# Kernel tuning notes

Hardware: AMD Instinct MI355X
Metric: run time of the kernel (lower is better)

Reference implementation:

```python
import jax, jax.numpy as jnp
import numpy as np

N = 100000   # nodes
E = 1600000  # edges
F_IN = 128   # node_features
H = 64       # hidden_features


def setup_inputs() -> dict:
    key = jax.random.key(0)
    ks = jax.random.split(key, 16)
    s = 0.05
    return {
        "x": jax.random.normal(ks[0], (N, F_IN), dtype=jnp.float32),
        "edge_index": jax.random.randint(ks[1], (2, E), 0, N, dtype=jnp.int64),
        "W1": jax.random.normal(ks[2], (H, F_IN), dtype=jnp.float32) * s,
        "b1": jnp.zeros((H,), dtype=jnp.float32),
        "W2": jax.random.normal(ks[3], (H, H), dtype=jnp.float32) * s,
        "b2": jnp.zeros((H,), dtype=jnp.float32),
        "Wk": jax.random.normal(ks[4], (H, H), dtype=jnp.float32) * s,
        "bk": jnp.zeros((H,), dtype=jnp.float32),
        "Wq": jax.random.normal(ks[5], (H, H), dtype=jnp.float32) * s,
        "bq": jnp.zeros((H,), dtype=jnp.float32),
        "Wv": jax.random.normal(ks[6], (H, H), dtype=jnp.float32) * s,
        "bv": jnp.zeros((H,), dtype=jnp.float32),
        "Ws": jax.random.normal(ks[7], (H, H), dtype=jnp.float32) * s,  # lin_skip, bias=False
        "b_gate": jnp.zeros((H,), dtype=jnp.float32),                   # conv bias param
        "Wsc": jax.random.normal(ks[8], (1, H), dtype=jnp.float32) * s,
        "bsc": jnp.zeros((1,), dtype=jnp.float32),
    }


def reference(x, edge_index, W1, b1, W2, b2, Wk, bk, Wq, bq, Wv, bv, Ws, b_gate, Wsc, bsc):
    # MLP front-end: Linear + ReLU + Linear
    h = jax.nn.relu(x @ W1.T + b1)
    h = h @ W2.T + b2                      # [N, H]

    # ResGatedGraphConv (sum aggregation, sigmoid gating)
    k = h @ Wk.T + bk                      # key on destination nodes
    q = h @ Wq.T + bq                      # query on source nodes
    v = h @ Wv.T + bv                      # value on source nodes

    src = edge_index[0]                    # j
    dst = edge_index[1]                    # i
    # message_ij = sigmoid(k_i + q_j) * v_j, scatter-add to destination i
    msg = jax.nn.sigmoid(k[dst] + q[src]) * v[src]   # [E, H]
    agg = jax.ops.segment_sum(msg, dst, num_segments=N)

    out = agg + h @ Ws.T + b_gate          # root skip (no bias) + conv bias

    # scorer head
    score = out @ Wsc.T + bsc              # [N, 1]
    return score
```

## Files before the change

### kernel.cpp

```cpp
#include <hip/hip_runtime.h>

#define HD  64
#define FIN 128

#define WS_W1H   0
#define WS_W1L   4096
#define WS_MALL  8192
#define WS_BK    14848
#define WS_BQ    14912
#define WS_BVW   14976
#define WS_BASE  15040
#define WS_REC   15104

#define C1f  3.9026344e-3f
#define C3f  (-7.67612e-8f)
#define C5f  1.2236660e-12f

typedef __attribute__((ext_vector_type(8))) short short8;
typedef __attribute__((ext_vector_type(4))) float f32x4;

__device__ __forceinline__ unsigned bf16rne(float f) {
    unsigned u = __float_as_uint(f);
    unsigned r = ((u >> 16) & 1u) + 0x7fffu;
    return (u + r) >> 16;
}
__device__ __forceinline__ float blo(unsigned u) { return __uint_as_float(u << 16); }
__device__ __forceinline__ float bhi(unsigned u) { return __uint_as_float(u & 0xffff0000u); }

__device__ __forceinline__ float grp4(unsigned ku, unsigned qu, unsigned va,
                                      unsigned vb, float p) {
    #pragma unroll
    for (int i = 0; i < 4; ++i) {
        float kf = (float)((ku >> (8 * i)) & 255u);
        float qf = (float)((qu >> (8 * i)) & 255u);
        unsigned vu = (i < 2) ? va : vb;
        float vf = (i & 1) ? bhi(vu) : blo(vu);
        float xx = kf + qf;
        xx = fminf(fmaxf(xx, 128.f), 384.f);
        float sv = xx - 256.f;
        float z = sv * sv;
        float w = fmaf(z, C5f, C3f);
        w = fmaf(z, w, C1f);
        p = fmaf(vf * sv, w, p);
        p = fmaf(vf, 0.5f, p);
    }
    return p;
}

__global__ void gnn_prep(const float* __restrict__ W1, const float* __restrict__ W2,
                         const float* __restrict__ b2,
                         const float* __restrict__ Wk, const float* __restrict__ bk,
                         const float* __restrict__ Wq, const float* __restrict__ bq,
                         const float* __restrict__ Wv, const float* __restrict__ bv,
                         const float* __restrict__ Wsm, const float* __restrict__ Wsc,
                         const float* __restrict__ bgate, const float* __restrict__ bsc,
                         float* __restrict__ ws) {
    __shared__ float w2s[4096];
    __shared__ float wxsT[65 * 64];
    int b = blockIdx.x, t = threadIdx.x;
    unsigned short* w1h  = (unsigned short*)(ws + WS_W1H);
    unsigned short* w1l  = (unsigned short*)(ws + WS_W1L);
    unsigned short* mall = (unsigned short*)(ws + WS_MALL);
    if (b == 0) {
        for (int idx = t; idx < HD * FIN; idx += blockDim.x) {
            float v = W1[idx];
            unsigned u = __float_as_uint(v);
            w1h[idx] = (unsigned short)(u >> 16);
            float rem = v - __uint_as_float(u & 0xffff0000u);
            w1l[idx] = (unsigned short)bf16rne(rem);
        }
    } else if (b <= 12) {
        int m = (b - 1) >> 2, qtr = (b - 1) & 3;
        const float* Wx = (m == 0) ? Wk : (m == 1) ? Wq : Wv;
        const float* bx = (m == 0) ? bk : (m == 1) ? bq : bv;
        int boff = (m == 0) ? WS_BK : (m == 1) ? WS_BQ : WS_BVW;
        for (int i = t * 4; i < 4096; i += 1024)
            *(float4*)&w2s[i] = *(const float4*)&W2[i];
        for (int idx = t; idx < 4096; idx += 256) {
            int o = idx >> 6, c = idx & 63;
            wxsT[c * 65 + o] = Wx[idx];
        }
        __syncthreads();
        for (int idx = t; idx < 1024; idx += 256) {
            int a = qtr * 16 + (idx >> 6), o = idx & 63;
            float acc = 0.f;
            for (int c = 0; c < HD; ++c) acc += w2s[c * HD + a] * wxsT[c * 65 + o];
            if (m == 2) acc *= Wsc[o];
            mall[(m * 64 + o) * HD + a] = (unsigned short)bf16rne(acc);
        }
        if (qtr == 0 && t < HD) {
            float acc = bx[t];
            for (int c = 0; c < HD; ++c) acc += b2[c] * wxsT[c * 65 + t];
            if (m == 2) acc *= Wsc[t];
            ws[boff + t] = acc;
        }
    } else {
        __shared__ float wsk[HD];
        if (t < HD) {
            float a = 0.f;
            for (int d = 0; d < HD; ++d) a += Wsm[d * HD + t] * Wsc[d];
            wsk[t] = a;
        }
        __syncthreads();
        if (t < HD) {
            float a = 0.f;
            for (int c = 0; c < HD; ++c) a += W2[c * HD + t] * wsk[c];
            mall[192 * HD + t] = (unsigned short)bf16rne(a);
        }
        for (int idx = t; idx < 15 * HD; idx += 256)
            mall[193 * HD + idx] = 0;
        if (t == 0) {
            float a = bsc[0];
            for (int d = 0; d < HD; ++d) a += bgate[d] * Wsc[d];
            float acc2 = 0.f;
            __syncthreads();
            for (int c = 0; c < HD; ++c) {
                float wk2 = 0.f;
                for (int d = 0; d < HD; ++d) wk2 += Wsm[d * HD + c] * Wsc[d];
                acc2 += b2[c] * wk2;
            }
            ws[WS_BASE] = a + acc2;
        }
    }
}

__global__ __launch_bounds__(256, 3) void gnn_node(const float* __restrict__ x,
                                                   const float* __restrict__ b1,
                                                   const float* __restrict__ ws,
                                                   unsigned* __restrict__ nodebuf,
                                                   float* __restrict__ score, int N) {
    __shared__ __align__(16) char smem[32768];
    char* XHb = smem;
    char* XLb = smem + 16384;

    int tid = threadIdx.x;
    int l = tid & 63, w = tid >> 6;
    int nbase = blockIdx.x * 64;

    #pragma unroll
    for (int it = 0; it < 8; ++it) {
        int idx = it * 64 + l;
        int nl = 16 * w + (idx >> 5);
        int c4 = idx & 31;
        int node = min(nbase + nl, N - 1);
        float4 v = ((const float4*)x)[(size_t)node * 32 + c4];
        unsigned u0 = __float_as_uint(v.x), u1 = __float_as_uint(v.y);
        unsigned u2 = __float_as_uint(v.z), u3 = __float_as_uint(v.w);
        uint2 hx, lx;
        hx.x = (u0 >> 16) | (u1 & 0xffff0000u);
        hx.y = (u2 >> 16) | (u3 & 0xffff0000u);
        float r0 = v.x - __uint_as_float(u0 & 0xffff0000u);
        float r1 = v.y - __uint_as_float(u1 & 0xffff0000u);
        float r2 = v.z - __uint_as_float(u2 & 0xffff0000u);
        float r3 = v.w - __uint_as_float(u3 & 0xffff0000u);
        lx.x = bf16rne(r0) | (bf16rne(r1) << 16);
        lx.y = bf16rne(r2) | (bf16rne(r3) << 16);
        int bo = (nl * 256 + c4 * 8) ^ ((nl & 7) << 4);
        *(uint2*)(XHb + bo) = hx;
        *(uint2*)(XLb + bo) = lx;
    }
    __syncthreads();

    int rl = l & 15, kb = l >> 4;
    int rowA = 16 * w + rl;
    int swzA = (rowA & 7) << 4;

    const unsigned short* w1h = (const unsigned short*)(ws + WS_W1H);
    const unsigned short* w1l = (const unsigned short*)(ws + WS_W1L);
    f32x4 acc1[4];
    #pragma unroll
    for (int t = 0; t < 4; ++t) {
        float bv = b1[t * 16 + rl];
        acc1[t] = (f32x4){bv, bv, bv, bv};
    }
    #pragma unroll
    for (int s = 0; s < 4; ++s) {
        int abyte = (rowA * 256 + s * 64 + kb * 16) ^ swzA;
        short8 ah = *(const short8*)(XHb + abyte);
        short8 al = *(const short8*)(XLb + abyte);
        int koff = s * 32 + kb * 8;
        #pragma unroll
        for (int t = 0; t < 4; ++t) {
            int col = t * 16 + rl;
            short8 bh = *(const short8*)&w1h[col * FIN + koff];
            short8 bl = *(const short8*)&w1l[col * FIN + koff];
            acc1[t] = __builtin_amdgcn_mfma_f32_16x16x32_bf16(ah, bh, acc1[t], 0, 0, 0);
            acc1[t] = __builtin_amdgcn_mfma_f32_16x16x32_bf16(al, bh, acc1[t], 0, 0, 0);
            acc1[t] = __builtin_amdgcn_mfma_f32_16x16x32_bf16(ah, bl, acc1[t], 0, 0, 0);
        }
    }
    __syncthreads();

    int r0w = (l >> 4) * 4;
    #pragma unroll
    for (int t = 0; t < 4; ++t) {
        int col = t * 16 + rl;
        #pragma unroll
        for (int r = 0; r < 4; ++r) {
            int row = 16 * w + r0w + r;
            float v = fmaxf(acc1[t][r], 0.f);
            int hb = (row * 128 + col * 2) ^ ((row & 7) << 4);
            *(unsigned short*)(smem + hb) = (unsigned short)bf16rne(v);
        }
    }
    __syncthreads();

    const unsigned short* mall = (const unsigned short*)(ws + WS_MALL);
    const float* bK = ws + WS_BK;
    const float* bQ = ws + WS_BQ;
    const float* bV = ws + WS_BVW;
    float base = ws[WS_BASE];
    f32x4 acc2[13];
    #pragma unroll
    for (int t = 0; t < 4; ++t) {
        float v = bK[t * 16 + rl];
        acc2[t] = (f32x4){v, v, v, v};
    }
    #pragma unroll
    for (int t = 0; t < 4; ++t) {
        float v = bQ[t * 16 + rl];
        acc2[4 + t] = (f32x4){v, v, v, v};
    }
    #pragma unroll
    for (int t = 0; t < 4; ++t) {
        float v = bV[t * 16 + rl];
        acc2[8 + t] = (f32x4){v, v, v, v};
    }
    acc2[12] = (f32x4){0.f, 0.f, 0.f, 0.f};

    #pragma unroll
    for (int s = 0; s < 2; ++s) {
        int abyte = (rowA * 128 + (s * 32 + kb * 8) * 2) ^ swzA;
        short8 a = *(const short8*)(smem + abyte);
        int koff = s * 32 + kb * 8;
        #pragma unroll
        for (int t = 0; t < 13; ++t) {
            short8 b = *(const short8*)&mall[(t * 16 + rl) * HD + koff];
            acc2[t] = __builtin_amdgcn_mfma_f32_16x16x32_bf16(a, b, acc2[t], 0, 0, 0);
        }
    }

    char* Ku = smem + 16384;
    char* Qu = smem + 20480;
    char* VW = smem + 24576;
    #pragma unroll
    for (int t = 0; t < 4; ++t) {
        int col = t * 16 + rl;
        #pragma unroll
        for (int r = 0; r < 4; ++r) {
            int row = 16 * w + r0w + r;
            int ek = min(max(__float2int_rn(fmaf(acc2[t][r],     64.f, 128.f)), 0), 255);
            int eq = min(max(__float2int_rn(fmaf(acc2[4 + t][r], 64.f, 128.f)), 0), 255);
            Ku[row * 64 + col] = (char)ek;
            Qu[row * 64 + col] = (char)eq;
            *(unsigned short*)(VW + row * 128 + col * 2) =
                (unsigned short)bf16rne(acc2[8 + t][r]);
        }
    }
    if (rl == 0) {
        #pragma unroll
        for (int r = 0; r < 4; ++r) {
            int node = nbase + 16 * w + r0w + r;
            if (node < N) score[node] = base + acc2[12][r];
        }
    }
    __syncthreads();

    uint4* recs = (uint4*)nodebuf;
    #pragma unroll
    for (int it = 0; it < 4; ++it) {
        int c = it * 256 + tid;
        int n = c >> 4, p = c & 15;
        uint4 v;
        if (p < 4)      v = *(const uint4*)(Ku + n * 64 + p * 16);
        else if (p < 8) v = *(const uint4*)(Qu + n * 64 + (p - 4) * 16);
        else            v = *(const uint4*)(VW + n * 128 + (p - 8) * 16);
        int node = nbase + n;
        if (node < N) recs[(size_t)node * 16 + p] = v;
    }
}

__global__ __launch_bounds__(256) void gnn_edge(const int* __restrict__ ei,
                                                const uint4* __restrict__ nb,
                                                float* __restrict__ score, int E) {
    int t = blockIdx.x * 256 + threadIdx.x;
    int e = t >> 2;
    if (e >= E) return;
    int f = t & 3;
    int s = ei[e];
    int d = ei[E + e];
    uint4 ku = nb[(size_t)d * 16 + f];
    uint4 qu = nb[(size_t)s * 16 + 4 + f];
    uint4 va = nb[(size_t)s * 16 + 8 + 2 * f];
    uint4 vb = nb[(size_t)s * 16 + 9 + 2 * f];
    float p = 0.f;
    p = grp4(ku.x, qu.x, va.x, va.y, p);
    p = grp4(ku.y, qu.y, va.z, va.w, p);
    p = grp4(ku.z, qu.z, vb.x, vb.y, p);
    p = grp4(ku.w, qu.w, vb.z, vb.w, p);
    p += __shfl_down(p, 2, 4);
    p += __shfl_down(p, 1, 4);
    if (f == 0) atomicAdd(&score[d], p);
}

extern "C" void kernel_launch(void* const* d_in, const int* in_sizes, int n_in,
                              void* d_out, int out_size, void* d_ws, size_t ws_size,
                              hipStream_t stream) {
    const float* x    = (const float*)d_in[0];
    const int*   ei   = (const int*)d_in[1];
    const float* W1   = (const float*)d_in[2];
    const float* b1   = (const float*)d_in[3];
    const float* W2   = (const float*)d_in[4];
    const float* b2   = (const float*)d_in[5];
    const float* Wk   = (const float*)d_in[6];
    const float* bk   = (const float*)d_in[7];
    const float* Wq   = (const float*)d_in[8];
    const float* bq   = (const float*)d_in[9];
    const float* Wv   = (const float*)d_in[10];
    const float* bv   = (const float*)d_in[11];
    const float* Wsm  = (const float*)d_in[12];
    const float* bgat = (const float*)d_in[13];
    const float* Wsc  = (const float*)d_in[14];
    const float* bsc  = (const float*)d_in[15];

    int N = in_sizes[0] / FIN;
    int E = in_sizes[1] / 2;

    float* ws    = (float*)d_ws;
    float* recs  = ws + WS_REC;
    float* score = (float*)d_out;

    int NB = (N + 63) / 64;
    gnn_prep<<<14, 256, 0, stream>>>(W1, W2, b2, Wk, bk, Wq, bq, Wv, bv,
                                     Wsm, Wsc, bgat, bsc, ws);
    gnn_node<<<NB, 256, 0, stream>>>(x, b1, ws, (unsigned*)recs, score, N);
    gnn_edge<<<(E * 4 + 255) / 256, 256, 0, stream>>>(ei, (const uint4*)recs, score, E);
}
```

Before: 294.3 us.

## Bucket edges by source block for L2-local gathers in edge kernel

Adds a per-call histogram, scan and scatter pass that groups edges into 32 buckets by source-node range (4096 nodes each), packing dst and local src into one 32-bit word. The edge kernel then walks the buckets with blocks interleaved so each XCD-like group of blocks touches a compact source range, meant to improve cache hit rates for the q/v gathers. Node records are split into separate K and QV arrays so the dst gather and src gather hit smaller arrays. This adds three extra kernels and extra traffic to read the edge list twice and write a packed buffer.

```diff
diff --git a/kernel.cpp b/kernel.cpp
--- a/kernel.cpp
+++ b/kernel.cpp
@@ -10,7 +10,12 @@
 #define WS_BQ    14912
 #define WS_BVW   14976
 #define WS_BASE  15040
-#define WS_REC   15104
+#define WS_CNT   15104
+#define WS_BOFF  15136
+#define WS_CUR   15172
+#define WS_K     15360
+
+#define BSHIFT 12
 
 #define C1f  3.9026344e-3f
 #define C3f  (-7.67612e-8f)
@@ -73,7 +78,7 @@
         int m = (b - 1) >> 2, qtr = (b - 1) & 3;
         const float* Wx = (m == 0) ? Wk : (m == 1) ? Wq : Wv;
         const float* bx = (m == 0) ? bk : (m == 1) ? bq : bv;
-        int boff = (m == 0) ? WS_BK : (m == 1) ? WS_BQ : WS_BVW;
+        int boffw = (m == 0) ? WS_BK : (m == 1) ? WS_BQ : WS_BVW;
         for (int i = t * 4; i < 4096; i += 1024)
             *(float4*)&w2s[i] = *(const float4*)&W2[i];
         for (int idx = t; idx < 4096; idx += 256) {
@@ -92,9 +97,9 @@
             float acc = bx[t];
             for (int c = 0; c < HD; ++c) acc += b2[c] * wxsT[c * 65 + t];
             if (m == 2) acc *= Wsc[t];
-            ws[boff + t] = acc;
-        }
-    } else {
+            ws[boffw + t] = acc;
+        }
+    } else if (b == 13) {
         __shared__ float wsk[HD];
         if (t < HD) {
             float a = 0.f;
@@ -113,7 +118,6 @@
             float a = bsc[0];
             for (int d = 0; d < HD; ++d) a += bgate[d] * Wsc[d];
             float acc2 = 0.f;
-            __syncthreads();
             for (int c = 0; c < HD; ++c) {
                 float wk2 = 0.f;
                 for (int d = 0; d < HD; ++d) wk2 += Wsm[d * HD + c] * Wsc[d];
@@ -121,13 +125,16 @@
             }
             ws[WS_BASE] = a + acc2;
         }
+    } else {
+        if (t < 128) ((int*)(ws + WS_CNT))[t] = 0;
     }
 }
 
 __global__ __launch_bounds__(256, 3) void gnn_node(const float* __restrict__ x,
                                                    const float* __restrict__ b1,
                                                    const float* __restrict__ ws,
-                                                   unsigned* __restrict__ nodebuf,
+                                                   uint4* __restrict__ karr,
+                                                   uint4* __restrict__ qv,
                                                    float* __restrict__ score, int N) {
     __shared__ __align__(16) char smem[32768];
     char* XHb = smem;
@@ -266,41 +273,115 @@
     }
     __syncthreads();
 
-    uint4* recs = (uint4*)nodebuf;
-    #pragma unroll
-    for (int it = 0; it < 4; ++it) {
-        int c = it * 256 + tid;
-        int n = c >> 4, p = c & 15;
-        uint4 v;
-        if (p < 4)      v = *(const uint4*)(Ku + n * 64 + p * 16);
-        else if (p < 8) v = *(const uint4*)(Qu + n * 64 + (p - 4) * 16);
-        else            v = *(const uint4*)(VW + n * 128 + (p - 8) * 16);
+    {
+        int n = tid >> 2, p = tid & 3;
         int node = nbase + n;
-        if (node < N) recs[(size_t)node * 16 + p] = v;
-    }
-}
-
-__global__ __launch_bounds__(256) void gnn_edge(const int* __restrict__ ei,
-                                                const uint4* __restrict__ nb,
-                                                float* __restrict__ score, int E) {
-    int t = blockIdx.x * 256 + threadIdx.x;
-    int e = t >> 2;
-    if (e >= E) return;
-    int f = t & 3;
-    int s = ei[e];
-    int d = ei[E + e];
-    uint4 ku = nb[(size_t)d * 16 + f];
-    uint4 qu = nb[(size_t)s * 16 + 4 + f];
-    uint4 va = nb[(size_t)s * 16 + 8 + 2 * f];
-    uint4 vb = nb[(size_t)s * 16 + 9 + 2 * f];
-    float p = 0.f;
-    p = grp4(ku.x, qu.x, va.x, va.y, p);
-    p = grp4(ku.y, qu.y, va.z, va.w, p);
-    p = grp4(ku.z, qu.z, vb.x, vb.y, p);
-    p = grp4(ku.w, qu.w, vb.z, vb.w, p);
-    p += __shfl_down(p, 2, 4);
-    p += __shfl_down(p, 1, 4);
-    if (f == 0) atomicAdd(&score[d], p);
+        if (node < N)
+            karr[(size_t)node * 4 + p] = *(const uint4*)(Ku + n * 64 + p * 16);
+    }
+    #pragma unroll
+    for (int it = 0; it < 3; ++it) {
+        int n = tid >> 2, p = (tid & 3) + it * 4;
+        int node = nbase + n;
+        const char* srcp = (p < 4) ? (Qu + n * 64 + p * 16)
+                                   : (VW + n * 128 + (p - 4) * 16);
+        if (node < N) qv[(size_t)node * 12 + p] = *(const uint4*)srcp;
+    }
+}
+
+__global__ __launch_bounds__(256) void gnn_hist(const int* __restrict__ ei,
+                                                int* __restrict__ cnt, int E) {
+    __shared__ int lc[32];
+    int t = threadIdx.x;
+    if (t < 32) lc[t] = 0;
+    __syncthreads();
+    for (int e = blockIdx.x * 256 + t; e < E; e += gridDim.x * 256)
+        atomicAdd(&lc[ei[e] >> BSHIFT], 1);
+    __syncthreads();
+    if (t < 32 && lc[t]) atomicAdd(&cnt[t], lc[t]);
+}
+
+__global__ void gnn_scan(const int* __restrict__ cnt, int* __restrict__ boff,
+                         int* __restrict__ cur) {
+    if (threadIdx.x == 0) {
+        int s = 0;
+        for (int b = 0; b < 32; ++b) { boff[b] = s; cur[b] = s; s += cnt[b]; }
+        boff[32] = s;
+    }
+}
+
+__global__ __launch_bounds__(256) void gnn_scatter(const int* __restrict__ ei,
+                                                   int* __restrict__ cur,
+                                                   unsigned* __restrict__ ebuf, int E) {
+    __shared__ int lc[32], gb[32], lcur[32];
+    int t = threadIdx.x;
+    int base = blockIdx.x * 1024;
+    if (t < 32) lc[t] = 0;
+    __syncthreads();
+    int myb[4]; unsigned mypk[4];
+    #pragma unroll
+    for (int i = 0; i < 4; ++i) {
+        int e = base + i * 256 + t;
+        myb[i] = -1;
+        if (e < E) {
+            int src = ei[e], dst = ei[E + e];
+            myb[i] = src >> BSHIFT;
+            mypk[i] = (unsigned)dst | ((unsigned)(src & 4095) << 17);
+            atomicAdd(&lc[myb[i]], 1);
+        }
+    }
+    __syncthreads();
+    if (t < 32) {
+        gb[t] = lc[t] ? atomicAdd(&cur[t], lc[t]) : 0;
+        lcur[t] = 0;
+    }
+    __syncthreads();
+    #pragma unroll
+    for (int i = 0; i < 4; ++i) {
+        if (myb[i] >= 0) {
+            int r = atomicAdd(&lcur[myb[i]], 1);
+            ebuf[gb[myb[i]] + r] = mypk[i];
+        }
+    }
+}
+
+__global__ __launch_bounds__(256) void gnn_edge(const unsigned* __restrict__ ebuf,
+                                                const int* __restrict__ boff,
+                                                const uint4* __restrict__ karr,
+                                                const uint4* __restrict__ qv,
+                                                float* __restrict__ score,
+                                                int nb, int cpb) {
+    int bid = blockIdx.x;
+    int x = bid & 7, ci = bid >> 3;
+    int t = threadIdx.x;
+    int q = t >> 2, f = t & 3;
+    for (int sb = 0; sb < 4; ++sb) {
+        int b = x + 8 * sb;
+        if (b >= nb) break;
+        int eend = boff[b + 1];
+        for (int c = ci; ; c += cpb) {
+            int e0 = boff[b] + c * 64;
+            if (e0 >= eend) break;
+            int ge = e0 + q;
+            if (ge < eend) {
+                unsigned pk = ebuf[ge];
+                int dst = (int)(pk & 0x1FFFFu);
+                int src = (b << BSHIFT) + (int)(pk >> 17);
+                uint4 ku = karr[(size_t)dst * 4 + f];
+                uint4 qu = qv[(size_t)src * 12 + f];
+                uint4 va = qv[(size_t)src * 12 + 4 + 2 * f];
+                uint4 vb = qv[(size_t)src * 12 + 5 + 2 * f];
+                float p = 0.f;
+                p = grp4(ku.x, qu.x, va.x, va.y, p);
+                p = grp4(ku.y, qu.y, va.z, va.w, p);
+                p = grp4(ku.z, qu.z, vb.x, vb.y, p);
+                p = grp4(ku.w, qu.w, vb.z, vb.w, p);
+                p += __shfl_down(p, 2, 4);
+                p += __shfl_down(p, 1, 4);
+                if (f == 0) atomicAdd(&score[dst], p);
+            }
+        }
+    }
 }
 
 extern "C" void kernel_launch(void* const* d_in, const int* in_sizes, int n_in,
@@ -327,12 +408,26 @@
     int E = in_sizes[1] / 2;
 
     float* ws    = (float*)d_ws;
-    float* recs  = ws + WS_REC;
+    int*   cnt   = (int*)(ws + WS_CNT);
+    int*   boff  = (int*)(ws + WS_BOFF);
+    int*   cur   = (int*)(ws + WS_CUR);
+    float* karr  = ws + WS_K;
+    float* qvarr = karr + (size_t)N * 16;
+    unsigned* ebuf = (unsigned*)(qvarr + (size_t)N * 48);
     float* score = (float*)d_out;
 
     int NB = (N + 63) / 64;
-    gnn_prep<<<14, 256, 0, stream>>>(W1, W2, b2, Wk, bk, Wq, bq, Wv, bv,
+    int nb = (N + (1 << BSHIFT) - 1) >> BSHIFT;
+    long long mean = ((long long)E << BSHIFT) / N;
+    int cpb = (int)(mean * 108 / 100 / 64) + 2;
+
+    gnn_prep<<<15, 256, 0, stream>>>(W1, W2, b2, Wk, bk, Wq, bq, Wv, bv,
                                      Wsm, Wsc, bgat, bsc, ws);
-    gnn_node<<<NB, 256, 0, stream>>>(x, b1, ws, (unsigned*)recs, score, N);
-    gnn_edge<<<(E * 4 + 255) / 256, 256, 0, stream>>>(ei, (const uint4*)recs, score, E);
-}
+    gnn_node<<<NB, 256, 0, stream>>>(x, b1, ws, (uint4*)karr, (uint4*)qvarr,
+                                     score, N);
+    gnn_hist<<<1024, 256, 0, stream>>>(ei, cnt, E);
+    gnn_scan<<<1, 64, 0, stream>>>(cnt, boff, cur);
+    gnn_scatter<<<(E + 1023) / 1024, 256, 0, stream>>>(ei, cur, ebuf, E);
+    gnn_edge<<<8 * cpb, 256, 0, stream>>>(ebuf, boff, (const uint4*)karr,
+                                          (const uint4*)qvarr, score, nb, cpb);
+}
```

New measurement: 332.7 us. 1.13x slower.

## Bucket edges by source block and stage source Q/V records in LDS

Applied to the files above, without the earlier changes.

Adds an edge-binning pass, fused into the node kernel as extra blocks, that scatters each edge into a per-128-source bucket with packed dst/local-src indices, plus a spill list for overflowing buckets. The edge kernel then loads each bucket's Q/V records into shared memory once and reads only K for the destination from global memory. The node output is split into separate K and QV arrays. The aim is to cut random global gathers of source features, at the cost of an extra atomic-based scatter pass and edge-buffer traffic.

```diff
diff --git a/kernel.cpp b/kernel.cpp
--- a/kernel.cpp
+++ b/kernel.cpp
@@ -10,7 +10,13 @@
 #define WS_BQ    14912
 #define WS_BVW   14976
 #define WS_BASE  15040
-#define WS_REC   15104
+#define WS_CUR   15104
+#define WS_K     16128
+
+#define BSHIFT 7
+#define BSIZE  128
+#define CAP    2368
+#define SPILLCAP 262144
 
 #define C1f  3.9026344e-3f
 #define C3f  (-7.67612e-8f)
@@ -54,7 +60,7 @@
                          const float* __restrict__ Wv, const float* __restrict__ bv,
                          const float* __restrict__ Wsm, const float* __restrict__ Wsc,
                          const float* __restrict__ bgate, const float* __restrict__ bsc,
-                         float* __restrict__ ws) {
+                         float* __restrict__ ws, int* __restrict__ cur) {
     __shared__ float w2s[4096];
     __shared__ float wxsT[65 * 64];
     int b = blockIdx.x, t = threadIdx.x;
@@ -73,7 +79,7 @@
         int m = (b - 1) >> 2, qtr = (b - 1) & 3;
         const float* Wx = (m == 0) ? Wk : (m == 1) ? Wq : Wv;
         const float* bx = (m == 0) ? bk : (m == 1) ? bq : bv;
-        int boff = (m == 0) ? WS_BK : (m == 1) ? WS_BQ : WS_BVW;
+        int boffw = (m == 0) ? WS_BK : (m == 1) ? WS_BQ : WS_BVW;
         for (int i = t * 4; i < 4096; i += 1024)
             *(float4*)&w2s[i] = *(const float4*)&W2[i];
         for (int idx = t; idx < 4096; idx += 256) {
@@ -92,9 +98,9 @@
             float acc = bx[t];
             for (int c = 0; c < HD; ++c) acc += b2[c] * wxsT[c * 65 + t];
             if (m == 2) acc *= Wsc[t];
-            ws[boff + t] = acc;
-        }
-    } else {
+            ws[boffw + t] = acc;
+        }
+    } else if (b == 13) {
         __shared__ float wsk[HD];
         if (t < HD) {
             float a = 0.f;
@@ -113,7 +119,6 @@
             float a = bsc[0];
             for (int d = 0; d < HD; ++d) a += bgate[d] * Wsc[d];
             float acc2 = 0.f;
-            __syncthreads();
             for (int c = 0; c < HD; ++c) {
                 float wk2 = 0.f;
                 for (int d = 0; d < HD; ++d) wk2 += Wsm[d * HD + c] * Wsc[d];
@@ -121,21 +126,47 @@
             }
             ws[WS_BASE] = a + acc2;
         }
-    }
-}
-
-__global__ __launch_bounds__(256, 3) void gnn_node(const float* __restrict__ x,
-                                                   const float* __restrict__ b1,
-                                                   const float* __restrict__ ws,
-                                                   unsigned* __restrict__ nodebuf,
-                                                   float* __restrict__ score, int N) {
+    } else {
+        for (int i = t; i < 1024; i += 256) cur[i] = 0;
+    }
+}
+
+__global__ __launch_bounds__(256, 3) void gnn_nodescatter(
+        const float* __restrict__ x, const float* __restrict__ b1,
+        const float* __restrict__ ws, uint4* __restrict__ karr,
+        uint4* __restrict__ qv, float* __restrict__ score, int N,
+        const int* __restrict__ ei, int* __restrict__ cur,
+        unsigned* __restrict__ ebuf, int* __restrict__ spillS,
+        int* __restrict__ spillD, int E, int NB, int nbkt) {
+    int tid = threadIdx.x;
+    int bid = blockIdx.x;
+
+    if (bid >= NB) {
+        int base = (bid - NB) * 1024;
+        #pragma unroll
+        for (int i = 0; i < 4; ++i) {
+            int e = base + i * 256 + tid;
+            if (e < E) {
+                int src = ei[e], dst = ei[E + e];
+                int b = src >> BSHIFT;
+                int r = atomicAdd(&cur[b], 1);
+                if (r < CAP)
+                    ebuf[(size_t)b * CAP + r] =
+                        (unsigned)dst | ((unsigned)(src & (BSIZE - 1)) << 17);
+                else {
+                    int sr = atomicAdd(&cur[nbkt], 1);
+                    if (sr < SPILLCAP) { spillS[sr] = src; spillD[sr] = dst; }
+                }
+            }
+        }
+        return;
+    }
+
     __shared__ __align__(16) char smem[32768];
     char* XHb = smem;
     char* XLb = smem + 16384;
-
-    int tid = threadIdx.x;
     int l = tid & 63, w = tid >> 6;
-    int nbase = blockIdx.x * 64;
+    int nbase = bid * 64;
 
     #pragma unroll
     for (int it = 0; it < 8; ++it) {
@@ -266,41 +297,87 @@
     }
     __syncthreads();
 
-    uint4* recs = (uint4*)nodebuf;
-    #pragma unroll
-    for (int it = 0; it < 4; ++it) {
-        int c = it * 256 + tid;
-        int n = c >> 4, p = c & 15;
-        uint4 v;
-        if (p < 4)      v = *(const uint4*)(Ku + n * 64 + p * 16);
-        else if (p < 8) v = *(const uint4*)(Qu + n * 64 + (p - 4) * 16);
-        else            v = *(const uint4*)(VW + n * 128 + (p - 8) * 16);
+    {
+        int n = tid >> 2, p = tid & 3;
         int node = nbase + n;
-        if (node < N) recs[(size_t)node * 16 + p] = v;
-    }
-}
-
-__global__ __launch_bounds__(256) void gnn_edge(const int* __restrict__ ei,
-                                                const uint4* __restrict__ nb,
-                                                float* __restrict__ score, int E) {
-    int t = blockIdx.x * 256 + threadIdx.x;
-    int e = t >> 2;
-    if (e >= E) return;
-    int f = t & 3;
-    int s = ei[e];
-    int d = ei[E + e];
-    uint4 ku = nb[(size_t)d * 16 + f];
-    uint4 qu = nb[(size_t)s * 16 + 4 + f];
-    uint4 va = nb[(size_t)s * 16 + 8 + 2 * f];
-    uint4 vb = nb[(size_t)s * 16 + 9 + 2 * f];
-    float p = 0.f;
-    p = grp4(ku.x, qu.x, va.x, va.y, p);
-    p = grp4(ku.y, qu.y, va.z, va.w, p);
-    p = grp4(ku.z, qu.z, vb.x, vb.y, p);
-    p = grp4(ku.w, qu.w, vb.z, vb.w, p);
-    p += __shfl_down(p, 2, 4);
-    p += __shfl_down(p, 1, 4);
-    if (f == 0) atomicAdd(&score[d], p);
+        if (node < N)
+            karr[(size_t)node * 4 + p] = *(const uint4*)(Ku + n * 64 + p * 16);
+    }
+    #pragma unroll
+    for (int it = 0; it < 3; ++it) {
+        int n = tid >> 2, p = (tid & 3) + it * 4;
+        int node = nbase + n;
+        const char* srcp = (p < 4) ? (Qu + n * 64 + p * 16)
+                                   : (VW + n * 128 + (p - 4) * 16);
+        if (node < N) qv[(size_t)node * 12 + p] = *(const uint4*)srcp;
+    }
+}
+
+__global__ __launch_bounds__(256, 4) void gnn_edge(const unsigned* __restrict__ ebuf,
+                                                   const int* __restrict__ cur,
+                                                   const uint4* __restrict__ karr,
+                                                   const uint4* __restrict__ qv,
+                                                   const int* __restrict__ spillS,
+                                                   const int* __restrict__ spillD,
+                                                   float* __restrict__ score,
+                                                   int nbkt, int N) {
+    int bid = blockIdx.x;
+    int tid = threadIdx.x;
+    int q = tid >> 2, f = tid & 3;
+
+    if (bid < 2 * nbkt) {
+        __shared__ uint4 lqv[BSIZE * 13];
+        int b = bid >> 1, h = bid & 1;
+        int gbase = b << BSHIFT;
+        #pragma unroll
+        for (int ch = 0; ch < 6; ++ch) {
+            int i = ch * 256 + tid;
+            int row = i / 12, p = i - row * 12;
+            int g = gbase + row;
+            if (g < N) lqv[row * 13 + p] = qv[(size_t)g * 12 + p];
+        }
+        __syncthreads();
+        int cnt = min(cur[b], CAP);
+        int chunks = (cnt + 63) >> 6;
+        for (int c = h; c < chunks; c += 2) {
+            int idx = c * 64 + q;
+            if (idx < cnt) {
+                unsigned pk = ebuf[(size_t)b * CAP + idx];
+                int dst = (int)(pk & 0x1FFFFu);
+                int sl = (int)(pk >> 17);
+                uint4 ku = karr[(size_t)dst * 4 + f];
+                uint4 qu = lqv[sl * 13 + f];
+                uint4 va = lqv[sl * 13 + 4 + 2 * f];
+                uint4 vb = lqv[sl * 13 + 5 + 2 * f];
+                float p = 0.f;
+                p = grp4(ku.x, qu.x, va.x, va.y, p);
+                p = grp4(ku.y, qu.y, va.z, va.w, p);
+                p = grp4(ku.z, qu.z, vb.x, vb.y, p);
+                p = grp4(ku.w, qu.w, vb.z, vb.w, p);
+                p += __shfl_down(p, 2, 4);
+                p += __shfl_down(p, 1, 4);
+                if (f == 0) atomicAdd(&score[dst], p);
+            }
+        }
+    } else {
+        int sc = min(cur[nbkt], SPILLCAP);
+        int sb = bid - 2 * nbkt;
+        for (int idx = sb * 64 + q; idx < sc; idx += 16 * 64) {
+            int src = spillS[idx], dst = spillD[idx];
+            uint4 ku = karr[(size_t)dst * 4 + f];
+            uint4 qu = qv[(size_t)src * 12 + f];
+            uint4 va = qv[(size_t)src * 12 + 4 + 2 * f];
+            uint4 vb = qv[(size_t)src * 12 + 5 + 2 * f];
+            float p = 0.f;
+            p = grp4(ku.x, qu.x, va.x, va.y, p);
+            p = grp4(ku.y, qu.y, va.z, va.w, p);
+            p = grp4(ku.z, qu.z, vb.x, vb.y, p);
+            p = grp4(ku.w, qu.w, vb.z, vb.w, p);
+            p += __shfl_down(p, 2, 4);
+            p += __shfl_down(p, 1, 4);
+            if (f == 0) atomicAdd(&score[dst], p);
+        }
+    }
 }
 
 extern "C" void kernel_launch(void* const* d_in, const int* in_sizes, int n_in,
@@ -326,13 +403,26 @@
     int N = in_sizes[0] / FIN;
     int E = in_sizes[1] / 2;
 
-    float* ws    = (float*)d_ws;
-    float* recs  = ws + WS_REC;
+    float* ws     = (float*)d_ws;
+    int*   cur    = (int*)(ws + WS_CUR);
+    float* karr   = ws + WS_K;
+    float* qvarr  = karr + (size_t)N * 16;
+    int nbkt = (N + BSIZE - 1) >> BSHIFT;
+    unsigned* ebuf = (unsigned*)(qvarr + (size_t)N * 48);
+    int* spillS = (int*)(ebuf + (size_t)nbkt * CAP);
+    int* spillD = spillS + SPILLCAP;
     float* score = (float*)d_out;
 
-    int NB = (N + 63) / 64;
-    gnn_prep<<<14, 256, 0, stream>>>(W1, W2, b2, Wk, bk, Wq, bq, Wv, bv,
-                                     Wsm, Wsc, bgat, bsc, ws);
-    gnn_node<<<NB, 256, 0, stream>>>(x, b1, ws, (unsigned*)recs, score, N);
-    gnn_edge<<<(E * 4 + 255) / 256, 256, 0, stream>>>(ei, (const uint4*)recs, score, E);
-}
+    int NB  = (N + 63) / 64;
+    int SCB = (E + 1023) / 1024;
+
+    gnn_prep<<<15, 256, 0, stream>>>(W1, W2, b2, Wk, bk, Wq, bq, Wv, bv,
+                                     Wsm, Wsc, bgat, bsc, ws, cur);
+    gnn_nodescatter<<<NB + SCB, 256, 0, stream>>>(x, b1, ws, (uint4*)karr,
+                                                  (uint4*)qvarr, score, N,
+                                                  ei, cur, ebuf, spillS, spillD,
+                                                  E, NB, nbkt);
+    gnn_edge<<<2 * nbkt + 16, 256, 0, stream>>>(ebuf, cur, (const uint4*)karr,
+                                                (const uint4*)qvarr, spillS,
+                                                spillD, score, nbkt, N);
+}
```

Result: slower. 663.3 us (+125.4%).
